# Kernel optimization log

Hardware: AMD Instinct MI355X
Metric: run time of the kernel (lower is better)

The kernel has to match this reference:

```python
import jax, jax.numpy as jnp
import numpy as np

B, I, H, L, D, O = 2048, 512, 512, 32, 1024, 512
TEMP = 1.0


def _make_params(key):
    ks = jax.random.split(key, 16)
    s = 0.05
    p = {}
    p['in_W'] = jax.random.normal(ks[0], (H, I), jnp.float32) * s
    p['in_b'] = jnp.zeros((H,), jnp.float32)
    p['out_W'] = jax.random.normal(ks[1], (O, H), jnp.float32) * s
    p['out_b'] = jnp.zeros((O,), jnp.float32)
    p['enc_Wih'] = jax.random.normal(ks[2], (4 * H, H), jnp.float32) * s
    p['enc_Whh'] = jax.random.normal(ks[3], (4 * H, H), jnp.float32) * s
    p['enc_bih'] = jnp.zeros((4 * H,), jnp.float32)
    p['enc_bhh'] = jnp.zeros((4 * H,), jnp.float32)
    p['dec_Wih'] = jax.random.normal(ks[4], (4 * H, H), jnp.float32) * s
    p['dec_Whh'] = jax.random.normal(ks[5], (4 * H, H), jnp.float32) * s
    p['dec_bih'] = jnp.zeros((4 * H,), jnp.float32)
    p['dec_bhh'] = jnp.zeros((4 * H,), jnp.float32)
    p['h2t_W'] = jax.random.normal(ks[6], (D, H), jnp.float32) * s
    p['h2t_b'] = jnp.zeros((D,), jnp.float32)
    p['t2h_W'] = jax.random.normal(ks[7], (H, D), jnp.float32) * s
    p['t2h_b'] = jnp.zeros((H,), jnp.float32)
    return p


def setup_inputs() -> dict:
    key = jax.random.key(0)
    k1, k2, k3 = jax.random.split(key, 3)
    inp = {'x': jax.random.normal(k1, (B, I), jnp.float32),
           'gumbel': jax.random.gumbel(k2, (L, B, D), jnp.float32)}
    inp.update(_make_params(k3))
    return inp


def _lstm_cell(x, h, c, Wih, Whh, bih, bhh):
    gates = x @ Wih.T + bih + h @ Whh.T + bhh  # [B, 4H]
    i, f, g, o = jnp.split(gates, 4, axis=-1)
    i = jax.nn.sigmoid(i); f = jax.nn.sigmoid(f)
    g = jnp.tanh(g); o = jax.nn.sigmoid(o)
    c_new = f * c + i * g
    h_new = o * jnp.tanh(c_new)
    return h_new, c_new


def reference(x, gumbel, in_W, in_b, out_W, out_b,
              enc_Wih, enc_Whh, enc_bih, enc_bhh,
              dec_Wih, dec_Whh, dec_bih, dec_bhh,
              h2t_W, h2t_b, t2h_W, t2h_b):
    # ---- encode ----
    x_emb = x @ in_W.T + in_b                      # [B, H]
    hx0 = jnp.zeros((B, H), x.dtype)
    inp0 = jnp.zeros((B, H), x.dtype)

    def enc_step(carry, g_noise):
        hx, cx, inp = carry
        hx, cx = _lstm_cell(inp, hx, cx, enc_Wih, enc_Whh, enc_bih, enc_bhh)
        pre = hx @ h2t_W.T + h2t_b                 # [B, D]
        soft = jax.nn.softmax((pre + g_noise) / TEMP, axis=-1)
        amax = jnp.argmax(soft, axis=-1)           # [B]
        oh = jax.nn.one_hot(amax, D, dtype=soft.dtype)
        z = soft + jax.lax.stop_gradient(oh - soft)  # straight-through
        inp = z @ t2h_W.T + t2h_b
        return (hx, cx, inp), (z, pre, amax)

    # initial cell state is the embedded input (cx = x), per the source
    _, (z_seq, logit_seq, msg_seq) = jax.lax.scan(
        enc_step, (hx0, x_emb, inp0), gumbel)
    one_hot = jnp.transpose(z_seq, (1, 0, 2))      # [B, L, D]
    logits = jnp.transpose(logit_seq, (1, 0, 2))   # [B, L, D]
    messages = msg_seq.T                           # [B, L]

    # ---- decode ----
    z_emb = z_seq @ t2h_W.T + t2h_b                # [L, B, H]

    def dec_step(carry, inp):
        hx, cx = carry
        hx, cx = _lstm_cell(inp, hx, cx, dec_Wih, dec_Whh, dec_bih, dec_bhh)
        return (hx, cx), None

    (hx_final, _), _ = jax.lax.scan(
        dec_step, (jnp.zeros((B, H), x.dtype), jnp.zeros((B, H), x.dtype)), z_emb)
    recon = hx_final @ out_W.T + out_b             # [B, O]
    return recon, one_hot, logits, messages
```

## Files before the change

kernel.cpp:

```cpp
#include <hip/hip_runtime.h>
#include <math.h>

#define B_  2048
#define I_  512
#define H_  512
#define L_  32
#define D_  1024
#define O_  512
#define H4_ 2048
#define KC  32

typedef _Float16 f16x8 __attribute__((ext_vector_type(8)));
typedef _Float16 f16x4 __attribute__((ext_vector_type(4)));
typedef float    f32x4 __attribute__((ext_vector_type(4)));

#define SPLIT_S  1024.0f
#define SPLIT_RS 0.0009765625f

__device__ __forceinline__ void gload16(const _Float16* g, _Float16* l) {
    __builtin_amdgcn_global_load_lds(
        (const __attribute__((address_space(1))) void*)g,
        (__attribute__((address_space(3))) void*)l, 16, 0, 0);
}

__device__ __forceinline__ f16x8 lds_frag(const _Float16* base, int row, int ko) {
    int off = row * 64 + ((((ko >> 3) ^ (row & 7))) << 3);
    return *(const f16x8*)(base + off);
}

__global__ __launch_bounds__(256) void gemm_atb(
    const float* __restrict__ A, const float* __restrict__ W,
    const float* __restrict__ bias, float* __restrict__ C, int ldc,
    float* __restrict__ C2, int ldc2,
    int M, int N, int K)
{
    __shared__ __align__(16) float As[KC][68];
    __shared__ __align__(16) float Ws[KC][68];
    const int tx = threadIdx.x & 15, ty = threadIdx.x >> 4;
    const int m0 = blockIdx.y * 64, n0 = blockIdx.x * 64;
    float acc[4][4] = {};

    for (int k0 = 0; k0 < K; k0 += KC) {
#pragma unroll
        for (int p = 0; p < 2; ++p) {
            int q = threadIdx.x + 256 * p;
            int r = q >> 3, c = q & 7;
            float4 va = *reinterpret_cast<const float4*>(
                &A[(long long)(m0 + r) * K + k0 + c * 4]);
            As[c * 4 + 0][r] = va.x; As[c * 4 + 1][r] = va.y;
            As[c * 4 + 2][r] = va.z; As[c * 4 + 3][r] = va.w;
            float4 vw = *reinterpret_cast<const float4*>(
                &W[(long long)(n0 + r) * K + k0 + c * 4]);
            Ws[c * 4 + 0][r] = vw.x; Ws[c * 4 + 1][r] = vw.y;
            Ws[c * 4 + 2][r] = vw.z; Ws[c * 4 + 3][r] = vw.w;
        }
        __syncthreads();
#pragma unroll
        for (int kk = 0; kk < KC; ++kk) {
            float4 a = *reinterpret_cast<const float4*>(&As[kk][ty * 4]);
            float4 w = *reinterpret_cast<const float4*>(&Ws[kk][tx * 4]);
            float av[4] = {a.x, a.y, a.z, a.w};
            float wv[4] = {w.x, w.y, w.z, w.w};
#pragma unroll
            for (int i = 0; i < 4; ++i)
#pragma unroll
                for (int j = 0; j < 4; ++j)
                    acc[i][j] = fmaf(av[i], wv[j], acc[i][j]);
        }
        __syncthreads();
    }

#pragma unroll
    for (int i = 0; i < 4; ++i) {
        int m = m0 + ty * 4 + i;
        int n = n0 + tx * 4;
        float4 out;
        out.x = acc[i][0]; out.y = acc[i][1]; out.z = acc[i][2]; out.w = acc[i][3];
        if (bias) {
            out.x += bias[n + 0]; out.y += bias[n + 1];
            out.z += bias[n + 2]; out.w += bias[n + 3];
        }
        *reinterpret_cast<float4*>(&C[(long long)m * ldc + n]) = out;
        if (C2)
            *reinterpret_cast<float4*>(&C2[(long long)m * ldc2 + n]) = out;
    }
}

__global__ __launch_bounds__(256) void split_f16(
    const float* __restrict__ src, _Float16* __restrict__ d1,
    _Float16* __restrict__ d2, int n4)
{
    int i = blockIdx.x * 256 + threadIdx.x;
    if (i >= n4) return;
    float4 v = reinterpret_cast<const float4*>(src)[i];
    float vv[4] = {v.x, v.y, v.z, v.w};
    f16x4 o1, o2;
#pragma unroll
    for (int j = 0; j < 4; ++j) {
        _Float16 hh = (_Float16)vv[j];
        o1[j] = hh;
        o2[j] = (_Float16)((vv[j] - (float)hh) * SPLIT_S);
    }
    *reinterpret_cast<f16x4*>(d1 + 4 * i) = o1;
    *reinterpret_cast<f16x4*>(d2 + 4 * i) = o2;
}

__global__ __launch_bounds__(256) void lstm_step_mfma(
    const _Float16* __restrict__ hx1, const _Float16* __restrict__ hx2,
    float* __restrict__ cx,
    const _Float16* __restrict__ W1, const _Float16* __restrict__ W2,
    const float* __restrict__ P,
    const int* __restrict__ m_prev,
    const float* __restrict__ bih, const float* __restrict__ bhh,
    _Float16* __restrict__ ho1, _Float16* __restrict__ ho2,
    float* __restrict__ hof)
{
    __shared__ __align__(16) _Float16 As1[64 * 64];
    __shared__ __align__(16) _Float16 As2[64 * 64];
    __shared__ __align__(16) _Float16 Ws1[128 * 64];
    __shared__ __align__(16) _Float16 Ws2[128 * 64];
    __shared__ int ms[64];

    const int tid = threadIdx.x;
    const int m0 = blockIdx.y * 64, h0 = blockIdx.x * 32;
    const int ln = tid & 63, wid = tid >> 6;
    const int wm = wid >> 1, wn = wid & 1;

    if (m_prev != nullptr && tid < 64) ms[tid] = m_prev[m0 + tid];

    f32x4 accM[2][4] = {};
    f32x4 accC[2][4] = {};

    for (int k0 = 0; k0 < H_; k0 += 64) {
        int jsw = ((ln & 7) ^ (ln >> 3)) << 3;
#pragma unroll
        for (int s = 0; s < 2; ++s) {
            int seg = wid + s * 4;
            int r   = seg * 8 + (ln >> 3);
            size_t ga = (size_t)(m0 + r) * H_ + k0 + jsw;
            gload16(hx1 + ga, &As1[seg * 512]);
            gload16(hx2 + ga, &As2[seg * 512]);
        }
#pragma unroll
        for (int s = 0; s < 4; ++s) {
            int seg = wid + s * 4;
            int r   = seg * 8 + (ln >> 3);
            int wrow = ((r >> 4) & 3) * H_ + h0 + ((r >> 6) << 4) + (r & 15);
            size_t gw = (size_t)wrow * H_ + k0 + jsw;
            gload16(W1 + gw, &Ws1[seg * 512]);
            gload16(W2 + gw, &Ws2[seg * 512]);
        }
        __syncthreads();
        const int ac = (ln >> 4) << 3;
        const int arow = wm * 32 + (ln & 15);
        const int brow = wn * 64 + (ln & 15);
#pragma unroll
        for (int kc = 0; kc < 2; ++kc) {
            int ko = kc * 32 + ac;
            f16x8 b1[4], b2[4];
#pragma unroll
            for (int fn = 0; fn < 4; ++fn) {
                b1[fn] = lds_frag(Ws1, brow + fn * 16, ko);
                b2[fn] = lds_frag(Ws2, brow + fn * 16, ko);
            }
#pragma unroll
            for (int fm = 0; fm < 2; ++fm) {
                f16x8 a1 = lds_frag(As1, arow + fm * 16, ko);
                f16x8 a2 = lds_frag(As2, arow + fm * 16, ko);
#pragma unroll
                for (int fn = 0; fn < 4; ++fn) {
                    accM[fm][fn] = __builtin_amdgcn_mfma_f32_16x16x32_f16(
                        a1, b1[fn], accM[fm][fn], 0, 0, 0);
                    accC[fm][fn] = __builtin_amdgcn_mfma_f32_16x16x32_f16(
                        a1, b2[fn], accC[fm][fn], 0, 0, 0);
                    accC[fm][fn] = __builtin_amdgcn_mfma_f32_16x16x32_f16(
                        a2, b1[fn], accC[fm][fn], 0, 0, 0);
                }
            }
        }
        __syncthreads();
    }

    const int hl = ln & 15;
    const int h  = h0 + wn * 16 + hl;
    const int rb = m0 + wm * 32 + ((ln >> 4) << 2);
    float bs0 = bih[0 * H_ + h] + bhh[0 * H_ + h];
    float bs1 = bih[1 * H_ + h] + bhh[1 * H_ + h];
    float bs2 = bih[2 * H_ + h] + bhh[2 * H_ + h];
    float bs3 = bih[3 * H_ + h] + bhh[3 * H_ + h];
#pragma unroll
    for (int fm = 0; fm < 2; ++fm) {
#pragma unroll
        for (int rg = 0; rg < 4; ++rg) {
            int b = rb + fm * 16 + rg;
            float g0 = accM[fm][0][rg] + SPLIT_RS * accC[fm][0][rg] + bs0;
            float g1 = accM[fm][1][rg] + SPLIT_RS * accC[fm][1][rg] + bs1;
            float g2 = accM[fm][2][rg] + SPLIT_RS * accC[fm][2][rg] + bs2;
            float g3 = accM[fm][3][rg] + SPLIT_RS * accC[fm][3][rg] + bs3;
            if (m_prev != nullptr) {
                const float* Pr = P + (size_t)ms[b - m0] * H4_;
                g0 += Pr[0 * H_ + h]; g1 += Pr[1 * H_ + h];
                g2 += Pr[2 * H_ + h]; g3 += Pr[3 * H_ + h];
            }
            float ig = 1.f / (1.f + expf(-g0));
            float fg = 1.f / (1.f + expf(-g1));
            float gg = tanhf(g2);
            float og = 1.f / (1.f + expf(-g3));
            size_t off = (size_t)b * H_ + h;
            float cnew = fg * cx[off] + ig * gg;
            cx[off] = cnew;
            float hv = og * tanhf(cnew);
            _Float16 hh1 = (_Float16)hv;
            ho1[off] = hh1;
            ho2[off] = (_Float16)((hv - (float)hh1) * SPLIT_S);
            if (hof != nullptr) hof[off] = hv;
        }
    }
}

__global__ __launch_bounds__(256) void gemm_pre_fused(
    const _Float16* __restrict__ A1, const _Float16* __restrict__ A2,
    const _Float16* __restrict__ W1, const _Float16* __restrict__ W2,
    const float* __restrict__ bias,
    float* __restrict__ C2, int ldc2,
    const float* __restrict__ gum,
    float* __restrict__ pbest, int* __restrict__ pidx)
{
    __shared__ __align__(16) _Float16 As1[64 * 64];
    __shared__ __align__(16) _Float16 As2[64 * 64];
    __shared__ __align__(16) _Float16 Ws1[64 * 64];
    __shared__ __align__(16) _Float16 Ws2[64 * 64];
    __shared__ float cb[2][64];
    __shared__ int   ci[2][64];

    const int tid = threadIdx.x;
    const int m0 = blockIdx.y * 64, n0 = blockIdx.x * 64;
    const int ln = tid & 63, wid = tid >> 6;
    const int wm = wid >> 1, wn = wid & 1;

    f32x4 accM[2][2] = {};
    f32x4 accC[2][2] = {};

    for (int k0 = 0; k0 < H_; k0 += 64) {
        int jsw = ((ln & 7) ^ (ln >> 3)) << 3;
#pragma unroll
        for (int s = 0; s < 2; ++s) {
            int seg = wid + s * 4;
            int r   = seg * 8 + (ln >> 3);
            size_t ga = (size_t)(m0 + r) * H_ + k0 + jsw;
            gload16(A1 + ga, &As1[seg * 512]);
            gload16(A2 + ga, &As2[seg * 512]);
        }
#pragma unroll
        for (int s = 0; s < 2; ++s) {
            int seg = wid + s * 4;
            int r   = seg * 8 + (ln >> 3);
            size_t gw = (size_t)(n0 + r) * H_ + k0 + jsw;
            gload16(W1 + gw, &Ws1[seg * 512]);
            gload16(W2 + gw, &Ws2[seg * 512]);
        }
        __syncthreads();
        const int ac = (ln >> 4) << 3;
        const int arow = wm * 32 + (ln & 15);
        const int brow = wn * 32 + (ln & 15);
#pragma unroll
        for (int kc = 0; kc < 2; ++kc) {
            int ko = kc * 32 + ac;
            f16x8 b1[2], b2[2];
#pragma unroll
            for (int fn = 0; fn < 2; ++fn) {
                b1[fn] = lds_frag(Ws1, brow + fn * 16, ko);
                b2[fn] = lds_frag(Ws2, brow + fn * 16, ko);
            }
#pragma unroll
            for (int fm = 0; fm < 2; ++fm) {
                f16x8 a1 = lds_frag(As1, arow + fm * 16, ko);
                f16x8 a2 = lds_frag(As2, arow + fm * 16, ko);
#pragma unroll
                for (int fn = 0; fn < 2; ++fn) {
                    accM[fm][fn] = __builtin_amdgcn_mfma_f32_16x16x32_f16(
                        a1, b1[fn], accM[fm][fn], 0, 0, 0);
                    accC[fm][fn] = __builtin_amdgcn_mfma_f32_16x16x32_f16(
                        a1, b2[fn], accC[fm][fn], 0, 0, 0);
                    accC[fm][fn] = __builtin_amdgcn_mfma_f32_16x16x32_f16(
                        a2, b1[fn], accC[fm][fn], 0, 0, 0);
                }
            }
        }
        __syncthreads();
    }

    const int hl = ln & 15;
    const int g4 = ln >> 4;
    const int rb = m0 + wm * 32 + (g4 << 2);
    float vbest[2][4]; int vidx[2][4];
#pragma unroll
    for (int fm = 0; fm < 2; ++fm)
#pragma unroll
        for (int rg = 0; rg < 4; ++rg) { vbest[fm][rg] = -INFINITY; vidx[fm][rg] = 0; }

#pragma unroll
    for (int fn = 0; fn < 2; ++fn) {
        int d = n0 + wn * 32 + fn * 16 + hl;
        float bv = bias[d];
#pragma unroll
        for (int fm = 0; fm < 2; ++fm)
#pragma unroll
            for (int rg = 0; rg < 4; ++rg) {
                int b = rb + fm * 16 + rg;
                float v = accM[fm][fn][rg] + SPLIT_RS * accC[fm][fn][rg] + bv;
                C2[(size_t)b * ldc2 + d] = v;
                float t = v + gum[(size_t)b * D_ + d];
                if (t > vbest[fm][rg]) { vbest[fm][rg] = t; vidx[fm][rg] = d; }
            }
    }

#pragma unroll
    for (int off = 1; off < 16; off <<= 1) {
#pragma unroll
        for (int fm = 0; fm < 2; ++fm)
#pragma unroll
            for (int rg = 0; rg < 4; ++rg) {
                float ov = __shfl_xor(vbest[fm][rg], off);
                int   oi = __shfl_xor(vidx[fm][rg], off);
                if (ov > vbest[fm][rg] ||
                    (ov == vbest[fm][rg] && oi < vidx[fm][rg])) {
                    vbest[fm][rg] = ov; vidx[fm][rg] = oi;
                }
            }
    }
    if (hl == 0) {
#pragma unroll
        for (int fm = 0; fm < 2; ++fm)
#pragma unroll
            for (int rg = 0; rg < 4; ++rg) {
                int rl = wm * 32 + fm * 16 + (g4 << 2) + rg;
                cb[wn][rl] = vbest[fm][rg];
                ci[wn][rl] = vidx[fm][rg];
            }
    }
    __syncthreads();
    if (tid < 64) {
        float b0 = cb[0][tid]; int i0 = ci[0][tid];
        float b1v = cb[1][tid]; int i1 = ci[1][tid];
        if (b1v > b0 || (b1v == b0 && i1 < i0)) { b0 = b1v; i0 = i1; }
        pbest[(size_t)(m0 + tid) * 16 + blockIdx.x] = b0;
        pidx [(size_t)(m0 + tid) * 16 + blockIdx.x] = i0;
    }
}

__global__ __launch_bounds__(256) void argmax_fin(
    const float* __restrict__ pbest, const int* __restrict__ pidx,
    float* __restrict__ onehot, float* __restrict__ messages,
    int* __restrict__ m_out, int l)
{
    int b = blockIdx.x * 256 + threadIdx.x;
    float best = -INFINITY; int bi = 0;
#pragma unroll
    for (int j = 0; j < 16; ++j) {
        float v = pbest[(size_t)b * 16 + j];
        int   i = pidx [(size_t)b * 16 + j];
        if (v > best || (v == best && i < bi)) { best = v; bi = i; }
    }
    m_out[b] = bi;
    messages[(size_t)b * L_ + l] = (float)bi;
    onehot[((size_t)b * L_ + l) * D_ + bi] = 1.0f;
}

__global__ __launch_bounds__(256) void build_emb(
    const float* __restrict__ t2h_W, const float* __restrict__ t2h_b,
    float* __restrict__ emb)
{
    int idx = blockIdx.x * 256 + threadIdx.x;
    int d = idx >> 9, h = idx & (H_ - 1);
    emb[idx] = t2h_W[(long long)h * D_ + d] + t2h_b[h];
}

extern "C" void kernel_launch(void* const* d_in, const int* in_sizes, int n_in,
                              void* d_out, int out_size, void* d_ws, size_t ws_size,
                              hipStream_t stream)
{
    (void)in_sizes; (void)n_in; (void)out_size; (void)ws_size;
    const float* x       = (const float*)d_in[0];
    const float* gumbel  = (const float*)d_in[1];
    const float* in_W    = (const float*)d_in[2];
    const float* in_b    = (const float*)d_in[3];
    const float* out_W   = (const float*)d_in[4];
    const float* out_b   = (const float*)d_in[5];
    const float* enc_Wih = (const float*)d_in[6];
    const float* enc_Whh = (const float*)d_in[7];
    const float* enc_bih = (const float*)d_in[8];
    const float* enc_bhh = (const float*)d_in[9];
    const float* dec_Wih = (const float*)d_in[10];
    const float* dec_Whh = (const float*)d_in[11];
    const float* dec_bih = (const float*)d_in[12];
    const float* dec_bhh = (const float*)d_in[13];
    const float* h2t_W   = (const float*)d_in[14];
    const float* h2t_b   = (const float*)d_in[15];
    const float* t2h_W   = (const float*)d_in[16];
    const float* t2h_b   = (const float*)d_in[17];

    float* out      = (float*)d_out;
    float* recon    = out;
    float* onehot   = out + (size_t)B_ * O_;
    float* logits   = onehot + (size_t)B_ * L_ * D_;
    float* messages = logits + (size_t)B_ * L_ * D_;

    float* ws    = (float*)d_ws;
    float* cx    = ws;
    float* emb   = cx + (size_t)B_ * H_;
    float* P_enc = emb + (size_t)D_ * H_;
    float* P_dec = P_enc + (size_t)D_ * H4_;
    float* hxf   = P_dec + (size_t)D_ * H4_;
    float* pbest = hxf + (size_t)B_ * H_;
    int*   pidx  = (int*)(pbest + (size_t)B_ * 16);
    int*   m_all = pidx + (size_t)B_ * 16;
    _Float16* fb   = (_Float16*)(m_all + (size_t)L_ * B_);
    _Float16* hxA1 = fb;  fb += (size_t)B_ * H_;
    _Float16* hxA2 = fb;  fb += (size_t)B_ * H_;
    _Float16* hxB1 = fb;  fb += (size_t)B_ * H_;
    _Float16* hxB2 = fb;  fb += (size_t)B_ * H_;
    _Float16* encW1 = fb; fb += (size_t)H4_ * H_;
    _Float16* encW2 = fb; fb += (size_t)H4_ * H_;
    _Float16* decW1 = fb; fb += (size_t)H4_ * H_;
    _Float16* decW2 = fb; fb += (size_t)H4_ * H_;
    _Float16* h2t1  = fb; fb += (size_t)D_ * H_;
    _Float16* h2t2  = fb;

    const dim3 blk256(256);

    (void)hipMemsetAsync(hxA1, 0, (size_t)B_ * H_ * 4, stream);
    (void)hipMemsetAsync(onehot, 0, (size_t)B_ * L_ * D_ * sizeof(float), stream);

    split_f16<<<dim3((H4_ * H_ / 4) / 256), blk256, 0, stream>>>(
        enc_Whh, encW1, encW2, H4_ * H_ / 4);
    split_f16<<<dim3((H4_ * H_ / 4) / 256), blk256, 0, stream>>>(
        dec_Whh, decW1, decW2, H4_ * H_ / 4);
    split_f16<<<dim3((D_ * H_ / 4) / 256), blk256, 0, stream>>>(
        h2t_W, h2t1, h2t2, D_ * H_ / 4);

    gemm_atb<<<dim3(H_ / 64, B_ / 64), blk256, 0, stream>>>(
        x, in_W, in_b, cx, H_, nullptr, 0, B_, H_, I_);

    build_emb<<<dim3((D_ * H_) / 256), blk256, 0, stream>>>(t2h_W, t2h_b, emb);
    gemm_atb<<<dim3(H4_ / 64, D_ / 64), blk256, 0, stream>>>(
        emb, enc_Wih, nullptr, P_enc, H4_, nullptr, 0, D_, H4_, H_);
    gemm_atb<<<dim3(H4_ / 64, D_ / 64), blk256, 0, stream>>>(
        emb, dec_Wih, nullptr, P_dec, H4_, nullptr, 0, D_, H4_, H_);

    _Float16 *c1 = hxA1, *c2 = hxA2, *n1 = hxB1, *n2 = hxB2;
    for (int l = 0; l < L_; ++l) {
        lstm_step_mfma<<<dim3(H_ / 32, B_ / 64), blk256, 0, stream>>>(
            c1, c2, cx, encW1, encW2, P_enc,
            (l == 0) ? nullptr : (m_all + (size_t)(l - 1) * B_),
            enc_bih, enc_bhh, n1, n2, nullptr);
        { _Float16* t = c1; c1 = n1; n1 = t; t = c2; c2 = n2; n2 = t; }
        gemm_pre_fused<<<dim3(D_ / 64, B_ / 64), blk256, 0, stream>>>(
            c1, c2, h2t1, h2t2, h2t_b,
            logits + (size_t)l * D_, L_ * D_,
            gumbel + (size_t)l * B_ * D_, pbest, pidx);
        argmax_fin<<<dim3(B_ / 256), blk256, 0, stream>>>(
            pbest, pidx, onehot, messages, m_all + (size_t)l * B_, l);
    }

    (void)hipMemsetAsync(c1, 0, (size_t)B_ * H_ * 2, stream);
    (void)hipMemsetAsync(c2, 0, (size_t)B_ * H_ * 2, stream);
    (void)hipMemsetAsync(cx, 0, (size_t)B_ * H_ * sizeof(float), stream);
    for (int l = 0; l < L_; ++l) {
        lstm_step_mfma<<<dim3(H_ / 32, B_ / 64), blk256, 0, stream>>>(
            c1, c2, cx, decW1, decW2, P_dec, m_all + (size_t)l * B_,
            dec_bih, dec_bhh, n1, n2, (l == L_ - 1) ? hxf : nullptr);
        { _Float16* t = c1; c1 = n1; n1 = t; t = c2; c2 = n2; n2 = t; }
    }

    gemm_atb<<<dim3(O_ / 64, B_ / 64), blk256, 0, stream>>>(
        hxf, out_W, out_b, recon, O_, nullptr, 0, B_, O_, H_);
}
```

Baseline: 2.873 ms.

## Interleave decoder LSTM steps with encoder steps and fuse argmax finalize

Runs each decoder LSTM step in the same launch as the next encoder step, using a z-dimension of 2 so the two recurrences share one grid. This doubles the parallelism per launch and removes the separate 32-step decoder loop. The argmax finalize kernel is folded into the LSTM kernel's gather prologue, and the P_enc/P_dec precompute GEMMs move to a split-f16 MFMA kernel. The cost is extra workspace for separate encoder and decoder state buffers and a more complex kernel with role-based pointer selection.

```diff
diff --git a/kernel.cpp b/kernel.cpp
--- a/kernel.cpp
+++ b/kernel.cpp
@@ -105,15 +105,102 @@
     *reinterpret_cast<f16x4*>(d2 + 4 * i) = o2;
 }
 
-__global__ __launch_bounds__(256) void lstm_step_mfma(
-    const _Float16* __restrict__ hx1, const _Float16* __restrict__ hx2,
-    float* __restrict__ cx,
+__global__ __launch_bounds__(256) void gemm_mfma_atb(
+    const _Float16* __restrict__ A1, const _Float16* __restrict__ A2,
     const _Float16* __restrict__ W1, const _Float16* __restrict__ W2,
-    const float* __restrict__ P,
-    const int* __restrict__ m_prev,
-    const float* __restrict__ bih, const float* __restrict__ bhh,
-    _Float16* __restrict__ ho1, _Float16* __restrict__ ho2,
-    float* __restrict__ hof)
+    float* __restrict__ C, int N, int K)
+{
+    __shared__ __align__(16) _Float16 As1[64 * 64];
+    __shared__ __align__(16) _Float16 As2[64 * 64];
+    __shared__ __align__(16) _Float16 Ws1[64 * 64];
+    __shared__ __align__(16) _Float16 Ws2[64 * 64];
+
+    const int tid = threadIdx.x;
+    const int m0 = blockIdx.y * 64, n0 = blockIdx.x * 64;
+    const int ln = tid & 63, wid = tid >> 6;
+    const int wm = wid >> 1, wn = wid & 1;
+
+    f32x4 accM[2][2] = {};
+    f32x4 accC[2][2] = {};
+
+    for (int k0 = 0; k0 < K; k0 += 64) {
+        int jsw = ((ln & 7) ^ (ln >> 3)) << 3;
+#pragma unroll
+        for (int s = 0; s < 2; ++s) {
+            int seg = wid + s * 4;
+            int r   = seg * 8 + (ln >> 3);
+            size_t ga = (size_t)(m0 + r) * K + k0 + jsw;
+            gload16(A1 + ga, &As1[seg * 512]);
+            gload16(A2 + ga, &As2[seg * 512]);
+            size_t gw = (size_t)(n0 + r) * K + k0 + jsw;
+            gload16(W1 + gw, &Ws1[seg * 512]);
+            gload16(W2 + gw, &Ws2[seg * 512]);
+        }
+        __syncthreads();
+        const int ac = (ln >> 4) << 3;
+        const int arow = wm * 32 + (ln & 15);
+        const int brow = wn * 32 + (ln & 15);
+#pragma unroll
+        for (int kc = 0; kc < 2; ++kc) {
+            int ko = kc * 32 + ac;
+            f16x8 b1[2], b2[2];
+#pragma unroll
+            for (int fn = 0; fn < 2; ++fn) {
+                b1[fn] = lds_frag(Ws1, brow + fn * 16, ko);
+                b2[fn] = lds_frag(Ws2, brow + fn * 16, ko);
+            }
+#pragma unroll
+            for (int fm = 0; fm < 2; ++fm) {
+                f16x8 a1 = lds_frag(As1, arow + fm * 16, ko);
+                f16x8 a2 = lds_frag(As2, arow + fm * 16, ko);
+#pragma unroll
+                for (int fn = 0; fn < 2; ++fn) {
+                    accM[fm][fn] = __builtin_amdgcn_mfma_f32_16x16x32_f16(
+                        a1, b1[fn], accM[fm][fn], 0, 0, 0);
+                    accC[fm][fn] = __builtin_amdgcn_mfma_f32_16x16x32_f16(
+                        a1, b2[fn], accC[fm][fn], 0, 0, 0);
+                    accC[fm][fn] = __builtin_amdgcn_mfma_f32_16x16x32_f16(
+                        a2, b1[fn], accC[fm][fn], 0, 0, 0);
+                }
+            }
+        }
+        __syncthreads();
+    }
+
+    const int hl = ln & 15;
+    const int rb = m0 + wm * 32 + ((ln >> 4) << 2);
+#pragma unroll
+    for (int fn = 0; fn < 2; ++fn) {
+        int d = n0 + wn * 32 + fn * 16 + hl;
+#pragma unroll
+        for (int fm = 0; fm < 2; ++fm)
+#pragma unroll
+            for (int rg = 0; rg < 4; ++rg) {
+                int b = rb + fm * 16 + rg;
+                C[(size_t)b * N + d] =
+                    accM[fm][fn][rg] + SPLIT_RS * accC[fm][fn][rg];
+            }
+    }
+}
+
+__global__ __launch_bounds__(256) void lstm_fused(
+    const _Float16* __restrict__ ehx1, const _Float16* __restrict__ ehx2,
+    float* __restrict__ ecx,
+    const _Float16* __restrict__ eW1, const _Float16* __restrict__ eW2,
+    const float* __restrict__ Pe,
+    const float* __restrict__ ebih, const float* __restrict__ ebhh,
+    _Float16* __restrict__ eho1, _Float16* __restrict__ eho2,
+    const _Float16* __restrict__ dhx1, const _Float16* __restrict__ dhx2,
+    float* __restrict__ dcx,
+    const _Float16* __restrict__ dW1, const _Float16* __restrict__ dW2,
+    const float* __restrict__ Pd,
+    const float* __restrict__ dbih, const float* __restrict__ dbhh,
+    _Float16* __restrict__ dho1, _Float16* __restrict__ dho2,
+    float* __restrict__ hof,
+    const float* __restrict__ pbest, const int* __restrict__ pidx,
+    int have_gather,
+    float* __restrict__ onehot, float* __restrict__ messages, int lmsg,
+    int encdec)
 {
     __shared__ __align__(16) _Float16 As1[64 * 64];
     __shared__ __align__(16) _Float16 As2[64 * 64];
@@ -125,8 +212,35 @@
     const int m0 = blockIdx.y * 64, h0 = blockIdx.x * 32;
     const int ln = tid & 63, wid = tid >> 6;
     const int wm = wid >> 1, wn = wid & 1;
-
-    if (m_prev != nullptr && tid < 64) ms[tid] = m_prev[m0 + tid];
+    const int role = (encdec == 3) ? (int)blockIdx.z : ((encdec & 1) ? 0 : 1);
+
+    const _Float16* hx1 = role ? dhx1 : ehx1;
+    const _Float16* hx2 = role ? dhx2 : ehx2;
+    float*          cx  = role ? dcx  : ecx;
+    const _Float16* W1  = role ? dW1  : eW1;
+    const _Float16* W2  = role ? dW2  : eW2;
+    const float*    P   = role ? Pd   : Pe;
+    const float*    bih = role ? dbih : ebih;
+    const float*    bhh = role ? dbhh : ebhh;
+    _Float16*       ho1 = role ? dho1 : eho1;
+    _Float16*       ho2 = role ? dho2 : eho2;
+
+    if (have_gather && tid < 64) {
+        int b = m0 + tid;
+        const float* pb = pbest + (size_t)b * 16;
+        const int*   pi = pidx  + (size_t)b * 16;
+        float best = -INFINITY; int bi = 0;
+#pragma unroll
+        for (int j = 0; j < 16; ++j) {
+            float v = pb[j]; int i = pi[j];
+            if (v > best || (v == best && i < bi)) { best = v; bi = i; }
+        }
+        ms[tid] = bi;
+        if (lmsg >= 0 && blockIdx.z == 0 && blockIdx.x == 0) {
+            messages[(size_t)b * L_ + lmsg] = (float)bi;
+            onehot[((size_t)b * L_ + lmsg) * D_ + bi] = 1.0f;
+        }
+    }
 
     f32x4 accM[2][4] = {};
     f32x4 accC[2][4] = {};
@@ -197,7 +311,7 @@
             float g1 = accM[fm][1][rg] + SPLIT_RS * accC[fm][1][rg] + bs1;
             float g2 = accM[fm][2][rg] + SPLIT_RS * accC[fm][2][rg] + bs2;
             float g3 = accM[fm][3][rg] + SPLIT_RS * accC[fm][3][rg] + bs3;
-            if (m_prev != nullptr) {
+            if (have_gather) {
                 const float* Pr = P + (size_t)ms[b - m0] * H4_;
                 g0 += Pr[0 * H_ + h]; g1 += Pr[1 * H_ + h];
                 g2 += Pr[2 * H_ + h]; g3 += Pr[3 * H_ + h];
@@ -213,7 +327,7 @@
             _Float16 hh1 = (_Float16)hv;
             ho1[off] = hh1;
             ho2[off] = (_Float16)((hv - (float)hh1) * SPLIT_S);
-            if (hof != nullptr) hof[off] = hv;
+            if (role && hof != nullptr) hof[off] = hv;
         }
     }
 }
@@ -347,24 +461,6 @@
         pbest[(size_t)(m0 + tid) * 16 + blockIdx.x] = b0;
         pidx [(size_t)(m0 + tid) * 16 + blockIdx.x] = i0;
     }
-}
-
-__global__ __launch_bounds__(256) void argmax_fin(
-    const float* __restrict__ pbest, const int* __restrict__ pidx,
-    float* __restrict__ onehot, float* __restrict__ messages,
-    int* __restrict__ m_out, int l)
-{
-    int b = blockIdx.x * 256 + threadIdx.x;
-    float best = -INFINITY; int bi = 0;
-#pragma unroll
-    for (int j = 0; j < 16; ++j) {
-        float v = pbest[(size_t)b * 16 + j];
-        int   i = pidx [(size_t)b * 16 + j];
-        if (v > best || (v == best && i < bi)) { best = v; bi = i; }
-    }
-    m_out[b] = bi;
-    messages[(size_t)b * L_ + l] = (float)bi;
-    onehot[((size_t)b * L_ + l) * D_ + bi] = 1.0f;
 }
 
 __global__ __launch_bounds__(256) void build_emb(
@@ -407,29 +503,41 @@
     float* messages = logits + (size_t)B_ * L_ * D_;
 
     float* ws    = (float*)d_ws;
-    float* cx    = ws;
-    float* emb   = cx + (size_t)B_ * H_;
+    float* ecx   = ws;
+    float* dcx   = ecx + (size_t)B_ * H_;
+    float* emb   = dcx + (size_t)B_ * H_;
     float* P_enc = emb + (size_t)D_ * H_;
     float* P_dec = P_enc + (size_t)D_ * H4_;
     float* hxf   = P_dec + (size_t)D_ * H4_;
     float* pbest = hxf + (size_t)B_ * H_;
     int*   pidx  = (int*)(pbest + (size_t)B_ * 16);
-    int*   m_all = pidx + (size_t)B_ * 16;
-    _Float16* fb   = (_Float16*)(m_all + (size_t)L_ * B_);
-    _Float16* hxA1 = fb;  fb += (size_t)B_ * H_;
-    _Float16* hxA2 = fb;  fb += (size_t)B_ * H_;
-    _Float16* hxB1 = fb;  fb += (size_t)B_ * H_;
-    _Float16* hxB2 = fb;  fb += (size_t)B_ * H_;
+    _Float16* fb   = (_Float16*)(pidx + (size_t)B_ * 16);
+    _Float16* ehA1 = fb;  fb += (size_t)B_ * H_;
+    _Float16* ehA2 = fb;  fb += (size_t)B_ * H_;
+    _Float16* ehB1 = fb;  fb += (size_t)B_ * H_;
+    _Float16* ehB2 = fb;  fb += (size_t)B_ * H_;
+    _Float16* dhA1 = fb;  fb += (size_t)B_ * H_;
+    _Float16* dhA2 = fb;  fb += (size_t)B_ * H_;
+    _Float16* dhB1 = fb;  fb += (size_t)B_ * H_;
+    _Float16* dhB2 = fb;  fb += (size_t)B_ * H_;
     _Float16* encW1 = fb; fb += (size_t)H4_ * H_;
     _Float16* encW2 = fb; fb += (size_t)H4_ * H_;
     _Float16* decW1 = fb; fb += (size_t)H4_ * H_;
     _Float16* decW2 = fb; fb += (size_t)H4_ * H_;
     _Float16* h2t1  = fb; fb += (size_t)D_ * H_;
-    _Float16* h2t2  = fb;
+    _Float16* h2t2  = fb; fb += (size_t)D_ * H_;
+    _Float16* embs1 = fb; fb += (size_t)D_ * H_;
+    _Float16* embs2 = fb; fb += (size_t)D_ * H_;
+    _Float16* eWih1 = fb; fb += (size_t)H4_ * H_;
+    _Float16* eWih2 = fb; fb += (size_t)H4_ * H_;
+    _Float16* dWih1 = fb; fb += (size_t)H4_ * H_;
+    _Float16* dWih2 = fb;
 
     const dim3 blk256(256);
 
-    (void)hipMemsetAsync(hxA1, 0, (size_t)B_ * H_ * 4, stream);
+    (void)hipMemsetAsync(ehA1, 0, (size_t)B_ * H_ * 4, stream);
+    (void)hipMemsetAsync(dhA1, 0, (size_t)B_ * H_ * 4, stream);
+    (void)hipMemsetAsync(dcx, 0, (size_t)B_ * H_ * sizeof(float), stream);
     (void)hipMemsetAsync(onehot, 0, (size_t)B_ * L_ * D_ * sizeof(float), stream);
 
     split_f16<<<dim3((H4_ * H_ / 4) / 256), blk256, 0, stream>>>(
@@ -438,40 +546,51 @@
         dec_Whh, decW1, decW2, H4_ * H_ / 4);
     split_f16<<<dim3((D_ * H_ / 4) / 256), blk256, 0, stream>>>(
         h2t_W, h2t1, h2t2, D_ * H_ / 4);
+    split_f16<<<dim3((H4_ * H_ / 4) / 256), blk256, 0, stream>>>(
+        enc_Wih, eWih1, eWih2, H4_ * H_ / 4);
+    split_f16<<<dim3((H4_ * H_ / 4) / 256), blk256, 0, stream>>>(
+        dec_Wih, dWih1, dWih2, H4_ * H_ / 4);
 
     gemm_atb<<<dim3(H_ / 64, B_ / 64), blk256, 0, stream>>>(
-        x, in_W, in_b, cx, H_, nullptr, 0, B_, H_, I_);
+        x, in_W, in_b, ecx, H_, nullptr, 0, B_, H_, I_);
 
     build_emb<<<dim3((D_ * H_) / 256), blk256, 0, stream>>>(t2h_W, t2h_b, emb);
-    gemm_atb<<<dim3(H4_ / 64, D_ / 64), blk256, 0, stream>>>(
-        emb, enc_Wih, nullptr, P_enc, H4_, nullptr, 0, D_, H4_, H_);
-    gemm_atb<<<dim3(H4_ / 64, D_ / 64), blk256, 0, stream>>>(
-        emb, dec_Wih, nullptr, P_dec, H4_, nullptr, 0, D_, H4_, H_);
-
-    _Float16 *c1 = hxA1, *c2 = hxA2, *n1 = hxB1, *n2 = hxB2;
+    split_f16<<<dim3((D_ * H_ / 4) / 256), blk256, 0, stream>>>(
+        emb, embs1, embs2, D_ * H_ / 4);
+    gemm_mfma_atb<<<dim3(H4_ / 64, D_ / 64), blk256, 0, stream>>>(
+        embs1, embs2, eWih1, eWih2, P_enc, H4_, H_);
+    gemm_mfma_atb<<<dim3(H4_ / 64, D_ / 64), blk256, 0, stream>>>(
+        embs1, embs2, dWih1, dWih2, P_dec, H4_, H_);
+
+    _Float16* e1[2] = {ehA1, ehB1};
+    _Float16* e2[2] = {ehA2, ehB2};
+    _Float16* d1[2] = {dhA1, dhB1};
+    _Float16* d2[2] = {dhA2, dhB2};
+
     for (int l = 0; l < L_; ++l) {
-        lstm_step_mfma<<<dim3(H_ / 32, B_ / 64), blk256, 0, stream>>>(
-            c1, c2, cx, encW1, encW2, P_enc,
-            (l == 0) ? nullptr : (m_all + (size_t)(l - 1) * B_),
-            enc_bih, enc_bhh, n1, n2, nullptr);
-        { _Float16* t = c1; c1 = n1; n1 = t; t = c2; c2 = n2; n2 = t; }
+        int ein = l & 1, eo = ein ^ 1;
+        int din = (l - 1) & 1, do_ = din ^ 1;
+        lstm_fused<<<dim3(H_ / 32, B_ / 64, l ? 2 : 1), blk256, 0, stream>>>(
+            e1[ein], e2[ein], ecx, encW1, encW2, P_enc, enc_bih, enc_bhh,
+            e1[eo], e2[eo],
+            l ? d1[din] : nullptr, l ? d2[din] : nullptr, dcx,
+            decW1, decW2, P_dec, dec_bih, dec_bhh,
+            l ? d1[do_] : nullptr, l ? d2[do_] : nullptr,
+            nullptr, pbest, pidx, l ? 1 : 0,
+            onehot, messages, l - 1, l ? 3 : 1);
         gemm_pre_fused<<<dim3(D_ / 64, B_ / 64), blk256, 0, stream>>>(
-            c1, c2, h2t1, h2t2, h2t_b,
+            e1[eo], e2[eo], h2t1, h2t2, h2t_b,
             logits + (size_t)l * D_, L_ * D_,
             gumbel + (size_t)l * B_ * D_, pbest, pidx);
-        argmax_fin<<<dim3(B_ / 256), blk256, 0, stream>>>(
-            pbest, pidx, onehot, messages, m_all + (size_t)l * B_, l);
-    }
-
-    (void)hipMemsetAsync(c1, 0, (size_t)B_ * H_ * 2, stream);
-    (void)hipMemsetAsync(c2, 0, (size_t)B_ * H_ * 2, stream);
-    (void)hipMemsetAsync(cx, 0, (size_t)B_ * H_ * sizeof(float), stream);
-    for (int l = 0; l < L_; ++l) {
-        lstm_step_mfma<<<dim3(H_ / 32, B_ / 64), blk256, 0, stream>>>(
-            c1, c2, cx, decW1, decW2, P_dec, m_all + (size_t)l * B_,
-            dec_bih, dec_bhh, n1, n2, (l == L_ - 1) ? hxf : nullptr);
-        { _Float16* t = c1; c1 = n1; n1 = t; t = c2; c2 = n2; n2 = t; }
-    }
+    }
+
+    lstm_fused<<<dim3(H_ / 32, B_ / 64, 1), blk256, 0, stream>>>(
+        nullptr, nullptr, ecx, encW1, encW2, P_enc, enc_bih, enc_bhh,
+        nullptr, nullptr,
+        d1[1], d2[1], dcx, decW1, decW2, P_dec, dec_bih, dec_bhh,
+        d1[0], d2[0],
+        hxf, pbest, pidx, 1,
+        onehot, messages, L_ - 1, 2);
 
     gemm_atb<<<dim3(O_ / 64, B_ / 64), blk256, 0, stream>>>(
         hxf, out_W, out_b, recon, O_, nullptr, 0, B_, O_, H_);
```

Measured after the change: 2.848 ms. Within noise of the previous version (-0.9%).
